# Performance work log

Measured on AMD Instinct MI355X. Metric: run time of the kernel, lower is better.

The kernel has to match this reference:

```python
import jax, jax.numpy as jnp
import numpy as np
from jax import lax

B, N, C = 4, 16384, 384
HEADS, HD = 8, 48
ALPHA = 4.0
KS = 5
HH = WW = 128


def setup_inputs() -> dict:
    key = jax.random.key(0)
    ks = jax.random.split(key, 9)
    s = 0.02
    return {
        "x": jax.random.normal(ks[0], (B, N, C), jnp.float32),
        "W_qg": jax.random.normal(ks[1], (C, 2 * C), jnp.float32) * s,
        "W_kv": jax.random.normal(ks[2], (C, 2 * C), jnp.float32) * s,
        "W_proj": jax.random.normal(ks[3], (C, C), jnp.float32) * s,
        "b_proj": jnp.zeros((C,), jnp.float32),
        "pos_enc": jax.random.normal(ks[4], (1, N, C), jnp.float32) * 0.02,
        "power_p": jax.random.normal(ks[5], (1, HEADS, 1, HD), jnp.float32) * 0.5,
        "scale_p": jax.random.normal(ks[6], (1, 1, C), jnp.float32) * 0.5,
        "dwc_w": jax.random.normal(ks[7], (HD, 1, KS, KS), jnp.float32) * s,
        "dwc_b": jnp.zeros((HD,), jnp.float32),
        "H": HH,
        "W": WW,
    }


def _relu_pow(x, p):
    # relu(x) ** p with safe gradients at x <= 0
    r = jax.nn.relu(x)
    base = jnp.where(r > 0, r, 1.0)
    return jnp.where(r > 0, base ** p, 0.0)


def reference(x, W_qg, W_kv, W_proj, b_proj, pos_enc, power_p, scale_p, dwc_w, dwc_b, H, W):
    Bx, Nx, Cx = x.shape
    h = power_p.shape[1]
    hd = power_p.shape[-1]

    qg = x @ W_qg                      # [B,N,2C]
    q, g = qg[..., :Cx], qg[..., Cx:]
    kv = x @ W_kv                      # [B,N,2C] (sr_ratio == 1)
    k, v = kv[..., :Cx], kv[..., Cx:]
    n = Nx
    k = k + pos_enc

    scale = jax.nn.softplus(scale_p)            # [1,1,C]
    power = 1.0 + ALPHA * jax.nn.sigmoid(power_p)  # [1,h,1,hd]
    q = q / scale
    k = k / scale

    # [B,h,N,hd]
    q = q.reshape(Bx, Nx, h, hd).transpose(0, 2, 1, 3)
    k = k.reshape(Bx, n, h, hd).transpose(0, 2, 1, 3)
    v = v.reshape(Bx, n, h, hd).transpose(0, 2, 1, 3)

    q_pos = _relu_pow(q, power)
    q_neg = _relu_pow(-q, power)
    k_pos = _relu_pow(k, power)
    k_neg = _relu_pow(-k, power)

    q_sim = jnp.concatenate([q_pos, q_neg], axis=-1)   # [B,h,N,2hd]
    q_opp = jnp.concatenate([q_neg, q_pos], axis=-1)
    kk = jnp.concatenate([k_pos, k_neg], axis=-1)      # [B,h,n,2hd]
    v1, v2 = v[..., : hd // 2], v[..., hd // 2:]

    k_mean = kk.mean(axis=2, keepdims=True)            # [B,h,1,2hd]
    inv_n = 1.0 / n

    z_sim = 1.0 / (jnp.sum(q_sim * k_mean, axis=-1, keepdims=True) + 1e-6)
    kv1 = jnp.einsum('bhnd,bhne->bhde', kk, v1) * inv_n  # [B,h,2hd,hd/2]
    x_sim = jnp.einsum('bhnd,bhde->bhne', q_sim, kv1) * z_sim

    z_opp = 1.0 / (jnp.sum(q_opp * k_mean, axis=-1, keepdims=True) + 1e-6)
    kv2 = jnp.einsum('bhnd,bhne->bhde', kk, v2) * inv_n
    x_opp = jnp.einsum('bhnd,bhde->bhne', q_opp, kv2) * z_opp

    out = jnp.concatenate([x_sim, x_opp], axis=-1)     # [B,h,N,hd]
    out = out.transpose(0, 2, 1, 3).reshape(Bx, Nx, Cx)

    # depthwise conv gate on v
    v4 = v.reshape(Bx * h, H, W, hd).transpose(0, 3, 1, 2)  # [B*h, hd, H, W]
    vc = lax.conv_general_dilated(
        v4, dwc_w, window_strides=(1, 1), padding='SAME',
        feature_group_count=hd,
        dimension_numbers=('NCHW', 'OIHW', 'NCHW'))
    vc = vc + dwc_b[None, :, None, None]
    v_out = vc.reshape(Bx, Cx, Nx).transpose(0, 2, 1)  # [B,N,C]

    out = (out + v_out) * g
    out = out @ W_proj + b_proj
    return out
```

## Files before the change

kernel.cpp:

```cpp
#include <hip/hip_runtime.h>
#include <math.h>


#define NB 4
#define NTOK 16384
#define CDIM 384
#define NHEAD 8
#define HDIM 48
#define IMGH 128
#define IMGW 128

typedef unsigned short u16;
typedef unsigned int u32;
typedef __attribute__((ext_vector_type(8))) short bf16x8;
typedef __attribute__((ext_vector_type(4))) float f32x4;

__device__ __forceinline__ float bf2f(u16 u) {
  return __uint_as_float(((unsigned)u) << 16);
}
__device__ __forceinline__ u16 f2bf(float f) {
  unsigned u = __float_as_uint(f);
  u += 0x7FFF + ((u >> 16) & 1);
  return (u16)(u >> 16);
}
__device__ __forceinline__ float pow_mag(float r, float p) {
  if (r < 1e-20f) return 0.0f;
  return exp2f(fminf(p * log2f(r), 80.0f));
}
__device__ __forceinline__ float ldx1(const void* p, size_t i, bool f32) {
  return f32 ? ((const float*)p)[i] : bf2f(((const u16*)p)[i]);
}
__device__ __forceinline__ void gload16(u16* lds, const u16* g) {
  __builtin_amdgcn_global_load_lds(
      (const __attribute__((address_space(1))) u32*)g,
      (__attribute__((address_space(3))) u32*)lds, 16, 0, 0);
}

__global__ __launch_bounds__(256) void k0_detect(const void* __restrict__ x,
                                                 int* __restrict__ flag) {
  __shared__ int s[256];
  const u16* p = (const u16*)x;
  const int t = threadIdx.x;
  int good = 0;
#pragma unroll
  for (int i = 0; i < 16; ++i) {
    const u16 w = p[t * 16 + i];
    const int e = (w >> 7) & 0xFF;
    good += (e >= 0x60 && e <= 0x85) ? 1 : 0;
  }
  s[t] = good;
  __syncthreads();
  for (int o = 128; o > 0; o >>= 1) {
    if (t < o) s[t] += s[t + o];
    __syncthreads();
  }
  if (t == 0) *flag = (s[0] >= (4096 * 4) / 5) ? 0 : 1;
}

__global__ __launch_bounds__(256) void kx_convert(const void* __restrict__ x,
                                                  const int* __restrict__ flag,
                                                  u16* __restrict__ xbf) {
  if (*flag == 0) return;
  const size_t S = (size_t)NB * NTOK * CDIM;
  const size_t tid = (size_t)blockIdx.x * 256 + threadIdx.x;
  const size_t stride = (size_t)gridDim.x * 256;
  const float4* xf = (const float4*)x;
  for (size_t i = tid; i < S / 8; i += stride) {
    const float4 a = xf[i * 2 + 0];
    const float4 b = xf[i * 2 + 1];
    *(ushort4*)(xbf + i * 8 + 0) = make_ushort4(f2bf(a.x), f2bf(a.y), f2bf(a.z), f2bf(a.w));
    *(ushort4*)(xbf + i * 8 + 4) = make_ushort4(f2bf(b.x), f2bf(b.y), f2bf(b.z), f2bf(b.w));
  }
}

__global__ __launch_bounds__(256) void kprep(
    const void* __restrict__ Wqg, const void* __restrict__ Wkv,
    const void* __restrict__ Wp, const int* __restrict__ flag,
    u16* __restrict__ W2T, u16* __restrict__ WpT)
{
  const bool f32 = (*flag != 0);
  const int idx = blockIdx.x * 256 + threadIdx.x;
  if (idx < 1536 * 384) {
    const int n = idx / 384, k = idx - n * 384;
    const float v = (n < 768) ? ldx1(Wqg, (size_t)k * 768 + n, f32)
                              : ldx1(Wkv, (size_t)k * 768 + (n - 768), f32);
    W2T[idx] = f2bf(v);
  } else {
    const int j = idx - 1536 * 384;
    if (j < 384 * 384) {
      const int n = j / 384, k = j - n * 384;
      WpT[j] = f2bf(ldx1(Wp, (size_t)k * 384 + n, f32));
    }
  }
}

__global__ __launch_bounds__(512) void k1_mfma(
    const void* __restrict__ x, const u16* __restrict__ xbf,
    const u16* __restrict__ W2T,
    const void* __restrict__ pos_enc, const void* __restrict__ scale_p,
    const int* __restrict__ flag, const int conv_ok,
    u16* __restrict__ qsT, u16* __restrict__ gT, u16* __restrict__ ksT, u16* __restrict__ vT)
{
  const bool f32 = (*flag != 0);
  const bool fast = (!f32) || (conv_ok != 0);
  const u16* Asrc = f32 ? xbf : (const u16*)x;
  __shared__ __align__(16) u16 smem[4][128 * 64];
  const int t = threadIdx.x;
  const int bid = blockIdx.x;
  const int rm = (bid & 7) * 768 + (bid >> 3);
  const int m_idx = rm / 12;
  const int n_idx = rm - m_idx * 12;
  const int n0 = n_idx * 128;
  const int m0 = m_idx * 128;
  const int wave = t >> 6, lane = t & 63;
  const int wr = wave >> 2, wc = wave & 3;
  const int lm = lane & 15, lq = lane >> 4;

  f32x4 acc[4][2] = {};

  auto STAGE = [&](int buf, int k0) {
#pragma unroll
    for (int i = 0; i < 2; ++i) {
      const int chunk = i * 512 + t;
      const int row = chunk >> 3, c8 = chunk & 7;
      const int sc8 = c8 ^ (row & 7);
      u16* lpA = &smem[buf][(i * 512 + wave * 64) * 8];
      u16* lpB = &smem[2 + buf][(i * 512 + wave * 64) * 8];
      gload16(lpA, Asrc + (size_t)(m0 + row) * CDIM + k0 + sc8 * 8);
      gload16(lpB, W2T + (size_t)(n0 + row) * CDIM + k0 + sc8 * 8);
    }
  };
  auto COMPUTE = [&](int buf) {
#pragma unroll
    for (int kh = 0; kh < 2; ++kh) {
      bf16x8 af[4], bfr[2];
#pragma unroll
      for (int r = 0; r < 4; ++r) {
        const int row = wr * 64 + r * 16 + lm;
        af[r] = *(const bf16x8*)&smem[buf][row * 64 + (((kh * 4 + lq) ^ (row & 7)) * 8)];
      }
#pragma unroll
      for (int cb = 0; cb < 2; ++cb) {
        const int row = wc * 32 + cb * 16 + lm;
        bfr[cb] = *(const bf16x8*)&smem[2 + buf][row * 64 + (((kh * 4 + lq) ^ (row & 7)) * 8)];
      }
#pragma unroll
      for (int r = 0; r < 4; ++r)
#pragma unroll
        for (int cb = 0; cb < 2; ++cb)
          acc[r][cb] = __builtin_amdgcn_mfma_f32_16x16x32_bf16(af[r], bfr[cb], acc[r][cb], 0, 0, 0);
    }
  };

  if (fast) {
    STAGE(0, 0);
    asm volatile("s_waitcnt vmcnt(0)" ::: "memory");
    __builtin_amdgcn_sched_barrier(0);
    __builtin_amdgcn_s_barrier();
    int cur = 0;
#pragma unroll
    for (int ks = 0; ks < 5; ++ks) {
      STAGE(cur ^ 1, (ks + 1) * 64);
      COMPUTE(cur);
      asm volatile("s_waitcnt vmcnt(0)" ::: "memory");
      __builtin_amdgcn_sched_barrier(0);
      __builtin_amdgcn_s_barrier();
      cur ^= 1;
    }
    COMPUTE(cur);
  } else {
    for (int k0 = 0; k0 < CDIM; k0 += 64) {
#pragma unroll
      for (int i = 0; i < 2; ++i) {
        const int chunk = t + i * 512;
        const int row = chunk >> 3, c8 = chunk & 7;
        const int ldsoff = row * 64 + ((c8 ^ (row & 7)) * 8);
        const float* xp = (const float*)x + (size_t)(m0 + row) * CDIM + k0 + c8 * 8;
        const float4 v0 = *(const float4*)xp;
        const float4 v1 = *(const float4*)(xp + 4);
        *(ushort4*)&smem[0][ldsoff]     = make_ushort4(f2bf(v0.x), f2bf(v0.y), f2bf(v0.z), f2bf(v0.w));
        *(ushort4*)&smem[0][ldsoff + 4] = make_ushort4(f2bf(v1.x), f2bf(v1.y), f2bf(v1.z), f2bf(v1.w));
        *(uint4*)&smem[2][ldsoff] = *(const uint4*)(W2T + (size_t)(n0 + row) * CDIM + k0 + c8 * 8);
      }
      __syncthreads();
      COMPUTE(0);
      __syncthreads();
    }
  }

  __syncthreads();
  u16* et = &smem[0][0];
  const int b = m0 >> 14;
  const int TOK0 = m0 & (NTOK - 1);
  const int region = n0 / CDIM;
#pragma unroll
  for (int cb = 0; cb < 2; ++cb) {
    const int cl = wc * 32 + cb * 16 + lm;
    const int c = (n0 - region * CDIM) + cl;
    float inv = 1.0f;
    if (region == 0 || region == 2) inv = 1.0f / log1pf(expf(ldx1(scale_p, c, f32)));
#pragma unroll
    for (int r = 0; r < 4; ++r) {
      const int tl = wr * 64 + r * 16 + lq * 4;
      const f32x4 v = acc[r][cb];
      ushort4 w;
      if (region == 2) {
        const int tok = TOK0 + tl;
        const float p0 = ldx1(pos_enc, (size_t)(tok + 0) * CDIM + c, f32);
        const float p1 = ldx1(pos_enc, (size_t)(tok + 1) * CDIM + c, f32);
        const float p2 = ldx1(pos_enc, (size_t)(tok + 2) * CDIM + c, f32);
        const float p3 = ldx1(pos_enc, (size_t)(tok + 3) * CDIM + c, f32);
        w = make_ushort4(f2bf((v[0] + p0) * inv), f2bf((v[1] + p1) * inv),
                         f2bf((v[2] + p2) * inv), f2bf((v[3] + p3) * inv));
      } else if (region == 0) {
        w = make_ushort4(f2bf(v[0] * inv), f2bf(v[1] * inv), f2bf(v[2] * inv), f2bf(v[3] * inv));
      } else {
        w = make_ushort4(f2bf(v[0]), f2bf(v[1]), f2bf(v[2]), f2bf(v[3]));
      }
      *(ushort4*)&et[cl * 136 + tl] = w;
    }
  }
  __syncthreads();
  u16* dst = (region == 0) ? qsT : (region == 1) ? gT : (region == 2) ? ksT : vT;
  const int cbase = b * CDIM + (n0 - region * CDIM);
#pragma unroll
  for (int i = 0; i < 4; ++i) {
    const int idx = i * 512 + t;
    const int row = idx >> 4, seg = idx & 15;
    const uint4 val = *(const uint4*)&et[row * 136 + seg * 8];
    *(uint4*)(dst + ((size_t)(cbase + row)) * NTOK + TOK0 + seg * 8) = val;
  }
}

__global__ __launch_bounds__(256) void k2_stats(
    const u16* __restrict__ ksT, const u16* __restrict__ vT,
    const void* __restrict__ power_p, const int* __restrict__ flag,
    float* __restrict__ km, float* __restrict__ kvm)
{
  const bool f32 = (*flag != 0);
  __shared__ float kkL[96][65];
  __shared__ float vL[48][65];
  __shared__ float pw[48];
  const int bh = blockIdx.x;
  const int b = bh >> 3, h = bh & 7;
  const int t = threadIdx.x;
  if (t < 48) pw[t] = 1.0f + 4.0f / (1.0f + expf(-ldx1(power_p, h * HDIM + t, f32)));
  __syncthreads();
  const int td = t & 15, te = t >> 4;
  float acc[6][3] = {};
  float ksum = 0.0f;
  const u16* ksbase = ksT + ((size_t)(b * CDIM + h * HDIM)) * NTOK;
  const u16* vbase  = vT  + ((size_t)(b * CDIM + h * HDIM)) * NTOK;
  const int n0base = blockIdx.y * 1024;
  for (int tile = 0; tile < 16; ++tile) {
    const int n0 = n0base + tile * 64;
    for (int i = t; i < 48 * 16; i += 256) {
      const int c = i >> 4, qd = (i & 15) * 4;
      ushort4 kq = *(const ushort4*)(ksbase + (size_t)c * NTOK + n0 + qd);
      ushort4 vq = *(const ushort4*)(vbase  + (size_t)c * NTOK + n0 + qd);
      const float p = pw[c];
      float kf[4] = {bf2f(kq.x), bf2f(kq.y), bf2f(kq.z), bf2f(kq.w)};
      float vf[4] = {bf2f(vq.x), bf2f(vq.y), bf2f(vq.z), bf2f(vq.w)};
#pragma unroll
      for (int jj = 0; jj < 4; ++jj) {
        const float f = pow_mag(fabsf(kf[jj]), p);
        kkL[c][qd + jj]      = (kf[jj] > 0.f) ? f : 0.f;
        kkL[c + 48][qd + jj] = (kf[jj] < 0.f) ? f : 0.f;
        vL[c][qd + jj] = vf[jj];
      }
    }
    __syncthreads();
#pragma unroll 2
    for (int nn = 0; nn < 64; ++nn) {
      float av[6], bv[3];
#pragma unroll
      for (int i = 0; i < 6; ++i) av[i] = kkL[td * 6 + i][nn];
#pragma unroll
      for (int j = 0; j < 3; ++j) bv[j] = vL[te * 3 + j][nn];
#pragma unroll
      for (int i = 0; i < 6; ++i)
#pragma unroll
        for (int j = 0; j < 3; ++j)
          acc[i][j] = fmaf(av[i], bv[j], acc[i][j]);
    }
    if (t < 96) {
#pragma unroll 4
      for (int nn = 0; nn < 64; ++nn) ksum += kkL[t][nn];
    }
    __syncthreads();
  }
  const float inv_n = 1.0f / (float)NTOK;
#pragma unroll
  for (int i = 0; i < 6; ++i)
#pragma unroll
    for (int j = 0; j < 3; ++j)
      atomicAdd(&kvm[(size_t)bh * 96 * 48 + (td * 6 + i) * 48 + (te * 3 + j)], acc[i][j] * inv_n);
  if (t < 96) atomicAdd(&km[bh * 96 + t], ksum * inv_n);
}

__global__ __launch_bounds__(256) void k3_attn(
    const u16* __restrict__ qsT, u16* __restrict__ attnT,
    const float* __restrict__ km_g, const float* __restrict__ kvm_g,
    const void* __restrict__ power_p, const int* __restrict__ flag)
{
  const bool f32 = (*flag != 0);
  __shared__ __align__(16) float kvmL[96][48];
  __shared__ float kmL[96];
  __shared__ float pw[48];
  const int bh = blockIdx.y;
  const int b = bh >> 3, h = bh & 7;
  const int t = threadIdx.x;
  for (int i = t; i < 96 * 48; i += 256) kvmL[i / 48][i % 48] = kvm_g[(size_t)bh * 96 * 48 + i];
  if (t < 96) kmL[t] = km_g[bh * 96 + t];
  if (t < 48) pw[t] = 1.0f + 4.0f / (1.0f + expf(-ldx1(power_p, h * HDIM + t, f32)));
  __syncthreads();
  const int n = blockIdx.x * 512 + t;
  const size_t chan0 = ((size_t)(b * CDIM + h * HDIM)) * NTOK + n;
  const u16* qbase = qsT + chan0;
  u16* obase = attnT + chan0;
  float4 accs[2][6] = {}, acco[2][6] = {};
  float zs[2] = {}, zo[2] = {};
  for (int d = 0; d < 48; ++d) {
    const float p = pw[d];
    float qp[2], qn[2];
#pragma unroll
    for (int i = 0; i < 2; ++i) {
      const float qv = bf2f(qbase[(size_t)d * NTOK + i * 256]);
      const float f = pow_mag(fabsf(qv), p);
      qp[i] = (qv > 0.f) ? f : 0.f;
      qn[i] = (qv < 0.f) ? f : 0.f;
      zs[i] = fmaf(qp[i], kmL[d], zs[i]); zs[i] = fmaf(qn[i], kmL[d + 48], zs[i]);
      zo[i] = fmaf(qn[i], kmL[d], zo[i]); zo[i] = fmaf(qp[i], kmL[d + 48], zo[i]);
    }
#pragma unroll
    for (int e4 = 0; e4 < 6; ++e4) {
      const float4 kvA = *(const float4*)&kvmL[d][e4 * 4];
      const float4 kvB = *(const float4*)&kvmL[d + 48][e4 * 4];
      const float4 kvC = *(const float4*)&kvmL[d][24 + e4 * 4];
      const float4 kvD = *(const float4*)&kvmL[d + 48][24 + e4 * 4];
#pragma unroll
      for (int i = 0; i < 2; ++i) {
        accs[i][e4].x = fmaf(qp[i], kvA.x, fmaf(qn[i], kvB.x, accs[i][e4].x));
        accs[i][e4].y = fmaf(qp[i], kvA.y, fmaf(qn[i], kvB.y, accs[i][e4].y));
        accs[i][e4].z = fmaf(qp[i], kvA.z, fmaf(qn[i], kvB.z, accs[i][e4].z));
        accs[i][e4].w = fmaf(qp[i], kvA.w, fmaf(qn[i], kvB.w, accs[i][e4].w));
        acco[i][e4].x = fmaf(qn[i], kvC.x, fmaf(qp[i], kvD.x, acco[i][e4].x));
        acco[i][e4].y = fmaf(qn[i], kvC.y, fmaf(qp[i], kvD.y, acco[i][e4].y));
        acco[i][e4].z = fmaf(qn[i], kvC.z, fmaf(qp[i], kvD.z, acco[i][e4].z));
        acco[i][e4].w = fmaf(qn[i], kvC.w, fmaf(qp[i], kvD.w, acco[i][e4].w));
      }
    }
  }
#pragma unroll
  for (int i = 0; i < 2; ++i) {
    const float zsi = 1.0f / (zs[i] + 1e-6f);
    const float zoi = 1.0f / (zo[i] + 1e-6f);
#pragma unroll
    for (int e4 = 0; e4 < 6; ++e4) {
      const float4 s = accs[i][e4], o = acco[i][e4];
      obase[(size_t)(e4 * 4 + 0) * NTOK + i * 256]    = f2bf(s.x * zsi);
      obase[(size_t)(e4 * 4 + 1) * NTOK + i * 256]    = f2bf(s.y * zsi);
      obase[(size_t)(e4 * 4 + 2) * NTOK + i * 256]    = f2bf(s.z * zsi);
      obase[(size_t)(e4 * 4 + 3) * NTOK + i * 256]    = f2bf(s.w * zsi);
      obase[(size_t)(24 + e4 * 4 + 0) * NTOK + i * 256] = f2bf(o.x * zoi);
      obase[(size_t)(24 + e4 * 4 + 1) * NTOK + i * 256] = f2bf(o.y * zoi);
      obase[(size_t)(24 + e4 * 4 + 2) * NTOK + i * 256] = f2bf(o.z * zoi);
      obase[(size_t)(24 + e4 * 4 + 3) * NTOK + i * 256] = f2bf(o.w * zoi);
    }
  }
}

__global__ __launch_bounds__(256) void k4_conv_combine(
    const u16* __restrict__ vT, const u16* __restrict__ gT,
    const void* __restrict__ dwc_w, const void* __restrict__ dwc_b,
    const int* __restrict__ flag,
    u16* __restrict__ attnT)
{
  const bool f32 = (*flag != 0);
  __shared__ float tile[20][128];
  const int bc = blockIdx.y;
  const int y0 = blockIdx.x * 16;
  const int t = threadIdx.x;
  const int d = bc % 48;
  float w[25];
#pragma unroll
  for (int i = 0; i < 25; ++i) w[i] = ldx1(dwc_w, d * 25 + i, f32);
  const float bias = ldx1(dwc_b, d, f32);
  const u16* vimg = vT + (size_t)bc * NTOK;
  for (int i = t; i < 20 * 128; i += 256) {
    const int r = i >> 7, xx = i & 127;
    const int gy = y0 + r - 2;
    tile[r][xx] = (gy >= 0 && gy < IMGH) ? bf2f(vimg[gy * IMGW + xx]) : 0.f;
  }
  __syncthreads();
  u16* abase = attnT + (size_t)bc * NTOK;
  const u16* gbase = gT + (size_t)bc * NTOK;
#pragma unroll
  for (int k = 0; k < 8; ++k) {
    const int px = t + k * 256;
    const int yy = px >> 7, xcol = px & 127;
    float acc = bias;
#pragma unroll
    for (int dy = 0; dy < 5; ++dy)
#pragma unroll
      for (int dx = 0; dx < 5; ++dx) {
        const int ux = xcol + dx - 2;
        const float val = (ux >= 0 && ux < IMGW) ? tile[yy + dy][ux] : 0.f;
        acc = fmaf(w[dy * 5 + dx], val, acc);
      }
    const int gidx = (y0 + yy) * IMGW + xcol;
    abase[gidx] = f2bf((bf2f(abase[gidx]) + acc) * bf2f(gbase[gidx]));
  }
}

__global__ __launch_bounds__(256) void k4b_transpose(
    const u16* __restrict__ src,
    u16* __restrict__ dst)
{
  __shared__ u16 tile[64][68];
  const int b  = blockIdx.z;
  const int c0 = blockIdx.y * 64;
  const int n0 = blockIdx.x * 64;
  const int t = threadIdx.x;
  const int tr = t >> 4, tq = t & 15;
#pragma unroll
  for (int i = 0; i < 4; ++i) {
    const int r = tr + i * 16;
    *(ushort4*)&tile[r][tq * 4] =
        *(const ushort4*)(src + ((size_t)(b * CDIM + c0 + r)) * NTOK + n0 + tq * 4);
  }
  __syncthreads();
#pragma unroll
  for (int i = 0; i < 4; ++i) {
    const int n = tr + i * 16;
    const ushort4 vv = make_ushort4(tile[tq * 4 + 0][n], tile[tq * 4 + 1][n],
                                    tile[tq * 4 + 2][n], tile[tq * 4 + 3][n]);
    *(ushort4*)(dst + ((size_t)(b * NTOK + n0 + n)) * CDIM + c0 + tq * 4) = vv;
  }
}

__global__ __launch_bounds__(256) void k5_mfma(
    const u16* __restrict__ A,
    const u16* __restrict__ WpT,
    const void* __restrict__ bp, const int* __restrict__ flag,
    void* __restrict__ out)
{
  const bool f32 = (*flag != 0);
  __shared__ __align__(16) u16 Asm[2][128 * 64];
  __shared__ __align__(16) u16 Bsm[2][128 * 64];
  const int t = threadIdx.x;
  const int bid = blockIdx.x;
  const int rm = (bid & 7) * 192 + (bid >> 3);
  const int m_idx = rm / 3;
  const int n_idx = rm - m_idx * 3;
  const int n0 = n_idx * 128;
  const int m0 = m_idx * 128;
  const int wave = t >> 6, lane = t & 63;
  const int wr = wave >> 1, wc = wave & 1;
  const int lm = lane & 15, lq = lane >> 4;

  f32x4 acc[4][4] = {};

  auto STAGE = [&](int buf, int k0) {
#pragma unroll
    for (int i = 0; i < 4; ++i) {
      const int chunk = i * 256 + t;
      const int row = chunk >> 3, c8 = chunk & 7;
      const int sc8 = c8 ^ (row & 7);
      u16* lpA = &Asm[buf][(i * 256 + wave * 64) * 8];
      u16* lpB = &Bsm[buf][(i * 256 + wave * 64) * 8];
      gload16(lpA, A + (size_t)(m0 + row) * CDIM + k0 + sc8 * 8);
      gload16(lpB, WpT + (size_t)(n0 + row) * CDIM + k0 + sc8 * 8);
    }
  };
  auto COMPUTE = [&](int buf) {
#pragma unroll
    for (int kh = 0; kh < 2; ++kh) {
      bf16x8 af[4], bfr[4];
#pragma unroll
      for (int r = 0; r < 4; ++r) {
        const int row = wr * 64 + r * 16 + lm;
        af[r] = *(const bf16x8*)&Asm[buf][row * 64 + (((kh * 4 + lq) ^ (row & 7)) * 8)];
      }
#pragma unroll
      for (int cb = 0; cb < 4; ++cb) {
        const int row = wc * 64 + cb * 16 + lm;
        bfr[cb] = *(const bf16x8*)&Bsm[buf][row * 64 + (((kh * 4 + lq) ^ (row & 7)) * 8)];
      }
#pragma unroll
      for (int r = 0; r < 4; ++r)
#pragma unroll
        for (int cb = 0; cb < 4; ++cb)
          acc[r][cb] = __builtin_amdgcn_mfma_f32_16x16x32_bf16(af[r], bfr[cb], acc[r][cb], 0, 0, 0);
    }
  };

  STAGE(0, 0);
  asm volatile("s_waitcnt vmcnt(0)" ::: "memory");
  __builtin_amdgcn_sched_barrier(0);
  __builtin_amdgcn_s_barrier();
  int cur = 0;
#pragma unroll
  for (int ks = 0; ks < 5; ++ks) {
    STAGE(cur ^ 1, (ks + 1) * 64);
    COMPUTE(cur);
    asm volatile("s_waitcnt vmcnt(0)" ::: "memory");
    __builtin_amdgcn_sched_barrier(0);
    __builtin_amdgcn_s_barrier();
    cur ^= 1;
  }
  COMPUTE(cur);

#pragma unroll
  for (int cb = 0; cb < 4; ++cb) {
    const int cg = n0 + wc * 64 + cb * 16 + lm;
    const float bb = ldx1(bp, cg, f32);
#pragma unroll
    for (int r = 0; r < 4; ++r) {
      const int rowtok = m0 + wr * 64 + r * 16 + lq * 4;
      const f32x4 v = acc[r][cb];
#pragma unroll
      for (int reg = 0; reg < 4; ++reg) {
        const size_t o = (size_t)(rowtok + reg) * CDIM + cg;
        if (f32) ((float*)out)[o] = v[reg] + bb;
        else     ((u16*)out)[o]   = f2bf(v[reg] + bb);
      }
    }
  }
}

extern "C" void kernel_launch(void* const* d_in, const int* in_sizes, int n_in,
                              void* d_out, int out_size, void* d_ws, size_t ws_size,
                              hipStream_t stream) {
  const void* x       = d_in[0];
  const void* Wqg     = d_in[1];
  const void* Wkv     = d_in[2];
  const void* Wproj   = d_in[3];
  const void* bproj   = d_in[4];
  const void* pos_enc = d_in[5];
  const void* power_p = d_in[6];
  const void* scale_p = d_in[7];
  const void* dwc_w   = d_in[8];
  const void* dwc_b   = d_in[9];

  const size_t S = (size_t)NB * NTOK * CDIM;
  const size_t stats_off   = 256;
  const size_t stats_bytes = (size_t)(32 * 96 + 32 * 96 * 48) * sizeof(float);
  const size_t w2t_elems = 1536 * 384, wpt_elems = 384 * 384;
  const size_t need = stats_off + stats_bytes + 3 * S * sizeof(u16)
                    + (w2t_elems + wpt_elems) * sizeof(u16);
  if (ws_size < need) return;

  int*   flag = (int*)d_ws;
  float* km   = (float*)((char*)d_ws + stats_off);
  float* kvm  = km + 32 * 96;
  u16* qsT = (u16*)((char*)d_ws + stats_off + stats_bytes);
  u16* gT  = qsT + S;
  u16* ksT = gT + S;
  u16* W2T = ksT + S;
  u16* WpT = W2T + w2t_elems;
  u16* vT  = (u16*)d_out;

  const int conv_ok = (out_size >= (int)(S * 4)) ? 1 : 0;
  u16* xbf = conv_ok ? ((u16*)d_out + S) : (u16*)d_out;

  hipMemsetAsync(km, 0, stats_bytes, stream);

  k0_detect<<<1, 256, 0, stream>>>(x, flag);
  if (conv_ok) kx_convert<<<2048, 256, 0, stream>>>(x, flag, xbf);
  kprep<<<(int)((w2t_elems + wpt_elems + 255) / 256), 256, 0, stream>>>(
      Wqg, Wkv, Wproj, flag, W2T, WpT);
  k1_mfma<<<6144, 512, 0, stream>>>(x, xbf, W2T, pos_enc, scale_p, flag, conv_ok,
                                    qsT, gT, ksT, vT);
  k2_stats<<<dim3(32, 16), 256, 0, stream>>>(ksT, vT, power_p, flag, km, kvm);
  k3_attn<<<dim3(32, 32), 256, 0, stream>>>(qsT, ksT, km, kvm, power_p, flag);
  k4_conv_combine<<<dim3(8, 1536), 256, 0, stream>>>(vT, gT, dwc_w, dwc_b, flag, ksT);
  k4b_transpose<<<dim3(256, 6, 4), 256, 0, stream>>>(ksT, qsT);
  k5_mfma<<<1536, 256, 0, stream>>>(qsT, WpT, bproj, flag, d_out);
}
```

Before: 787.9 us.

## Replace double-buffered LDS pipeline with single-buffer synchronous staging in GEMM kernels

Both MFMA GEMM kernels (the QG/KV projection and the output projection) drop the two-stage LDS double buffer and its manual waitcnt/barrier schedule. Each K-step now loads a tile, syncs, computes, and syncs again. This halves LDS use per block, which could allow more resident blocks per CU. The cost is that global loads no longer overlap MFMA compute within a block, and the loop is no longer forced unrolled.

```diff
diff --git a/kernel.cpp b/kernel.cpp
--- a/kernel.cpp
+++ b/kernel.cpp
@@ -104,7 +104,9 @@
   const bool f32 = (*flag != 0);
   const bool fast = (!f32) || (conv_ok != 0);
   const u16* Asrc = f32 ? xbf : (const u16*)x;
-  __shared__ __align__(16) u16 smem[4][128 * 64];
+  __shared__ __align__(16) u16 smem[17408];
+  u16* Asm = smem;
+  u16* Bsm = smem + 8192;
   const int t = threadIdx.x;
   const int bid = blockIdx.x;
   const int rm = (bid & 7) * 768 + (bid >> 3);
@@ -118,31 +120,31 @@
 
   f32x4 acc[4][2] = {};
 
-  auto STAGE = [&](int buf, int k0) {
+  auto STAGE = [&](int k0) {
 #pragma unroll
     for (int i = 0; i < 2; ++i) {
       const int chunk = i * 512 + t;
       const int row = chunk >> 3, c8 = chunk & 7;
       const int sc8 = c8 ^ (row & 7);
-      u16* lpA = &smem[buf][(i * 512 + wave * 64) * 8];
-      u16* lpB = &smem[2 + buf][(i * 512 + wave * 64) * 8];
+      u16* lpA = &Asm[(i * 512 + wave * 64) * 8];
+      u16* lpB = &Bsm[(i * 512 + wave * 64) * 8];
       gload16(lpA, Asrc + (size_t)(m0 + row) * CDIM + k0 + sc8 * 8);
       gload16(lpB, W2T + (size_t)(n0 + row) * CDIM + k0 + sc8 * 8);
     }
   };
-  auto COMPUTE = [&](int buf) {
+  auto COMPUTE = [&]() {
 #pragma unroll
     for (int kh = 0; kh < 2; ++kh) {
       bf16x8 af[4], bfr[2];
 #pragma unroll
       for (int r = 0; r < 4; ++r) {
         const int row = wr * 64 + r * 16 + lm;
-        af[r] = *(const bf16x8*)&smem[buf][row * 64 + (((kh * 4 + lq) ^ (row & 7)) * 8)];
+        af[r] = *(const bf16x8*)&Asm[row * 64 + (((kh * 4 + lq) ^ (row & 7)) * 8)];
       }
 #pragma unroll
       for (int cb = 0; cb < 2; ++cb) {
         const int row = wc * 32 + cb * 16 + lm;
-        bfr[cb] = *(const bf16x8*)&smem[2 + buf][row * 64 + (((kh * 4 + lq) ^ (row & 7)) * 8)];
+        bfr[cb] = *(const bf16x8*)&Bsm[row * 64 + (((kh * 4 + lq) ^ (row & 7)) * 8)];
       }
 #pragma unroll
       for (int r = 0; r < 4; ++r)
@@ -153,21 +155,12 @@
   };
 
   if (fast) {
-    STAGE(0, 0);
-    asm volatile("s_waitcnt vmcnt(0)" ::: "memory");
-    __builtin_amdgcn_sched_barrier(0);
-    __builtin_amdgcn_s_barrier();
-    int cur = 0;
-#pragma unroll
-    for (int ks = 0; ks < 5; ++ks) {
-      STAGE(cur ^ 1, (ks + 1) * 64);
-      COMPUTE(cur);
-      asm volatile("s_waitcnt vmcnt(0)" ::: "memory");
-      __builtin_amdgcn_sched_barrier(0);
-      __builtin_amdgcn_s_barrier();
-      cur ^= 1;
-    }
-    COMPUTE(cur);
+    for (int ks = 0; ks < 6; ++ks) {
+      STAGE(ks * 64);
+      __syncthreads();
+      COMPUTE();
+      __syncthreads();
+    }
   } else {
     for (int k0 = 0; k0 < CDIM; k0 += 64) {
 #pragma unroll
@@ -178,18 +171,17 @@
         const float* xp = (const float*)x + (size_t)(m0 + row) * CDIM + k0 + c8 * 8;
         const float4 v0 = *(const float4*)xp;
         const float4 v1 = *(const float4*)(xp + 4);
-        *(ushort4*)&smem[0][ldsoff]     = make_ushort4(f2bf(v0.x), f2bf(v0.y), f2bf(v0.z), f2bf(v0.w));
-        *(ushort4*)&smem[0][ldsoff + 4] = make_ushort4(f2bf(v1.x), f2bf(v1.y), f2bf(v1.z), f2bf(v1.w));
-        *(uint4*)&smem[2][ldsoff] = *(const uint4*)(W2T + (size_t)(n0 + row) * CDIM + k0 + c8 * 8);
+        *(ushort4*)&Asm[ldsoff]     = make_ushort4(f2bf(v0.x), f2bf(v0.y), f2bf(v0.z), f2bf(v0.w));
+        *(ushort4*)&Asm[ldsoff + 4] = make_ushort4(f2bf(v1.x), f2bf(v1.y), f2bf(v1.z), f2bf(v1.w));
+        *(uint4*)&Bsm[ldsoff] = *(const uint4*)(W2T + (size_t)(n0 + row) * CDIM + k0 + c8 * 8);
       }
       __syncthreads();
-      COMPUTE(0);
+      COMPUTE();
       __syncthreads();
     }
   }
 
-  __syncthreads();
-  u16* et = &smem[0][0];
+  u16* et = smem;
   const int b = m0 >> 14;
   const int TOK0 = m0 & (NTOK - 1);
   const int region = n0 / CDIM;
@@ -446,8 +438,8 @@
     void* __restrict__ out)
 {
   const bool f32 = (*flag != 0);
-  __shared__ __align__(16) u16 Asm[2][128 * 64];
-  __shared__ __align__(16) u16 Bsm[2][128 * 64];
+  __shared__ __align__(16) u16 Asm[128 * 64];
+  __shared__ __align__(16) u16 Bsm[128 * 64];
   const int t = threadIdx.x;
   const int bid = blockIdx.x;
   const int rm = (bid & 7) * 192 + (bid >> 3);
@@ -461,31 +453,31 @@
 
   f32x4 acc[4][4] = {};
 
-  auto STAGE = [&](int buf, int k0) {
+  auto STAGE = [&](int k0) {
 #pragma unroll
     for (int i = 0; i < 4; ++i) {
       const int chunk = i * 256 + t;
       const int row = chunk >> 3, c8 = chunk & 7;
       const int sc8 = c8 ^ (row & 7);
-      u16* lpA = &Asm[buf][(i * 256 + wave * 64) * 8];
-      u16* lpB = &Bsm[buf][(i * 256 + wave * 64) * 8];
+      u16* lpA = &Asm[(i * 256 + wave * 64) * 8];
+      u16* lpB = &Bsm[(i * 256 + wave * 64) * 8];
       gload16(lpA, A + (size_t)(m0 + row) * CDIM + k0 + sc8 * 8);
       gload16(lpB, WpT + (size_t)(n0 + row) * CDIM + k0 + sc8 * 8);
     }
   };
-  auto COMPUTE = [&](int buf) {
+  auto COMPUTE = [&]() {
 #pragma unroll
     for (int kh = 0; kh < 2; ++kh) {
       bf16x8 af[4], bfr[4];
 #pragma unroll
       for (int r = 0; r < 4; ++r) {
         const int row = wr * 64 + r * 16 + lm;
-        af[r] = *(const bf16x8*)&Asm[buf][row * 64 + (((kh * 4 + lq) ^ (row & 7)) * 8)];
+        af[r] = *(const bf16x8*)&Asm[row * 64 + (((kh * 4 + lq) ^ (row & 7)) * 8)];
       }
 #pragma unroll
       for (int cb = 0; cb < 4; ++cb) {
         const int row = wc * 64 + cb * 16 + lm;
-        bfr[cb] = *(const bf16x8*)&Bsm[buf][row * 64 + (((kh * 4 + lq) ^ (row & 7)) * 8)];
+        bfr[cb] = *(const bf16x8*)&Bsm[row * 64 + (((kh * 4 + lq) ^ (row & 7)) * 8)];
       }
 #pragma unroll
       for (int r = 0; r < 4; ++r)
@@ -495,21 +487,12 @@
     }
   };
 
-  STAGE(0, 0);
-  asm volatile("s_waitcnt vmcnt(0)" ::: "memory");
-  __builtin_amdgcn_sched_barrier(0);
-  __builtin_amdgcn_s_barrier();
-  int cur = 0;
-#pragma unroll
-  for (int ks = 0; ks < 5; ++ks) {
-    STAGE(cur ^ 1, (ks + 1) * 64);
-    COMPUTE(cur);
-    asm volatile("s_waitcnt vmcnt(0)" ::: "memory");
-    __builtin_amdgcn_sched_barrier(0);
-    __builtin_amdgcn_s_barrier();
-    cur ^= 1;
-  }
-  COMPUTE(cur);
+  for (int ks = 0; ks < 6; ++ks) {
+    STAGE(ks * 64);
+    __syncthreads();
+    COMPUTE();
+    __syncthreads();
+  }
 
 #pragma unroll
   for (int cb = 0; cb < 4; ++cb) {
```

Result: no change. 794.6 us (+0.9%).
